# Performance work log

Hardware: AMD Instinct MI355X
Metric: run time of the kernel (lower is better)

The kernel has to match this reference:

```python
import jax, jax.numpy as jnp
import numpy as np

NUM_HEADS = 16
KEY_DIM = 64
B, S, D = 2, 2048, 1024


def setup_inputs() -> dict:
    key = jax.random.key(0)
    ks = jax.random.split(key, 5)
    scale = 1.0 / np.sqrt(D)
    return {
        "x": jax.random.normal(ks[0], (B, S, D), dtype=jnp.float32),
        "Wq": jax.random.normal(ks[1], (D, NUM_HEADS * KEY_DIM), dtype=jnp.float32) * scale,
        "Wk": jax.random.normal(ks[2], (D, NUM_HEADS * KEY_DIM), dtype=jnp.float32) * scale,
        "Wv": jax.random.normal(ks[3], (D, NUM_HEADS * KEY_DIM), dtype=jnp.float32) * scale,
        "Wo": jax.random.normal(ks[4], (NUM_HEADS * KEY_DIM, D), dtype=jnp.float32) * scale,
    }


def reference(x, Wq, Wk, Wv, Wo):
    b, s, d = x.shape
    h, kd = NUM_HEADS, KEY_DIM
    # QKV projections -> [B, H, S, Kd]
    q = (x @ Wq).reshape(b, s, h, kd).transpose(0, 2, 1, 3)
    k = (x @ Wk).reshape(b, s, h, kd).transpose(0, 2, 1, 3)
    v = (x @ Wv).reshape(b, s, h, kd).transpose(0, 2, 1, 3)
    # scaled dot-product attention, full [B,H,S,S] scores (faithful to source)
    logits = jnp.einsum("bhqd,bhkd->bhqk", q, k) / jnp.sqrt(jnp.float32(kd))
    attn = jax.nn.softmax(logits, axis=-1)
    out = jnp.einsum("bhqk,bhkd->bhqd", attn, v)  # [B,H,S,Kd]
    out = out.transpose(0, 2, 1, 3).reshape(b, s, h * kd)
    return out @ Wo
```

## Files before the change

### kernel.cpp

```cpp
#include <hip/hip_runtime.h>


typedef __attribute__((ext_vector_type(8))) short short8;
typedef __attribute__((ext_vector_type(4))) float f32x4;

#define M_ROWS 4096
#define N_COLS 1024
#define K_DIM  1024
#define SEQ    2048

#define QSCALE 0.18033688011111772f

#if defined(__has_builtin)
#if __has_builtin(__builtin_amdgcn_exp2f)
#define EXP2(x) __builtin_amdgcn_exp2f(x)
#endif
#endif
#ifndef EXP2
#define EXP2(x) exp2f(x)
#endif

#define WAITCNT_VM8 0x0F78
#define WAITCNT_VM4 0x0F74

__device__ inline unsigned short f2bf(float f) {
  unsigned int u = __float_as_uint(f);
  u += 0x7fffu + ((u >> 16) & 1u);
  return (unsigned short)(u >> 16);
}

__device__ inline unsigned int pack2bf(float a, float b) {
  unsigned int ua = __float_as_uint(a); ua += 0x7fffu + ((ua >> 16) & 1u);
  unsigned int ub = __float_as_uint(b); ub += 0x7fffu + ((ub >> 16) & 1u);
  return (ua >> 16) | (ub & 0xffff0000u);
}

__device__ inline unsigned int cvtpk(float lo, float hi) {
  unsigned int r;
  asm("v_cvt_pk_bf16_f32 %0, %1, %2" : "=v"(r) : "v"(lo), "v"(hi));
  return r;
}

__device__ inline void swap32(unsigned int& a, unsigned int& b) {
  asm volatile("v_permlane32_swap_b32 %0, %1" : "+v"(a), "+v"(b));
}
__device__ inline void swap16(unsigned int& a, unsigned int& b) {
  asm volatile("v_permlane16_swap_b32 %0, %1" : "+v"(a), "+v"(b));
}

__device__ inline void async_load16(const unsigned short* gptr, unsigned short* lptr) {
  __builtin_amdgcn_global_load_lds(
      (const __attribute__((address_space(1))) unsigned int*)gptr,
      (__attribute__((address_space(3))) unsigned int*)lptr, 16, 0, 0);
}

__global__ void detect_kernel(const unsigned short* __restrict__ x, int* __restrict__ flag) {
  __shared__ int bad;
  if (threadIdx.x == 0) bad = 0;
  __syncthreads();
  for (int i = threadIdx.x; i < 1024; i += 256) {
    float f = __uint_as_float((unsigned int)x[i] << 16);
    float a = fabsf(f);
    if (!(a < 1e4f)) atomicOr(&bad, 1);
  }
  __syncthreads();
  if (threadIdx.x == 0) *flag = bad ? 0 : 1;
}

__global__ void convert_kernel(const void* __restrict__ src, unsigned short* __restrict__ dst,
                               int n4, const int* __restrict__ flag) {
  const int isbf = *flag;
  const int stride = gridDim.x * blockDim.x;
  for (int i = blockIdx.x * blockDim.x + threadIdx.x; i < n4; i += stride) {
    if (isbf) {
      ((uint2*)dst)[i] = ((const uint2*)src)[i];
    } else {
      float4 v = ((const float4*)src)[i];
      ushort4 o;
      o.x = f2bf(v.x); o.y = f2bf(v.y); o.z = f2bf(v.z); o.w = f2bf(v.w);
      ((ushort4*)dst)[i] = o;
    }
  }
}

__global__ __launch_bounds__(256) void convert_wT4_kernel(
    const void* __restrict__ s0, const void* __restrict__ s1,
    const void* __restrict__ s2, const void* __restrict__ s3,
    unsigned short* __restrict__ d0, unsigned short* __restrict__ d1,
    unsigned short* __restrict__ d2, unsigned short* __restrict__ d3,
    const int* __restrict__ flag) {
  __shared__ unsigned short t[32][33];
  const int z = blockIdx.z;
  const void* src = (z == 0) ? s0 : (z == 1) ? s1 : (z == 2) ? s2 : s3;
  unsigned short* dst = (z == 0) ? d0 : (z == 1) ? d1 : (z == 2) ? d2 : d3;
  const int tid = threadIdx.x;
  const int r0 = blockIdx.y * 32, c0 = blockIdx.x * 32;
  const int kr = tid >> 3, nc = (tid & 7) * 4;
  if (*flag) {
    const unsigned short* W = (const unsigned short*)src;
    uint2 v = *(const uint2*)(W + (size_t)(r0 + kr) * K_DIM + c0 + nc);
    t[kr][nc] = v.x & 0xffff; t[kr][nc + 1] = v.x >> 16;
    t[kr][nc + 2] = v.y & 0xffff; t[kr][nc + 3] = v.y >> 16;
  } else {
    const float* W = (const float*)src;
    float4 v = *(const float4*)(W + (size_t)(r0 + kr) * K_DIM + c0 + nc);
    t[kr][nc] = f2bf(v.x); t[kr][nc + 1] = f2bf(v.y);
    t[kr][nc + 2] = f2bf(v.z); t[kr][nc + 3] = f2bf(v.w);
  }
  __syncthreads();
  const int nr = tid >> 3, kc = (tid & 7) * 4;
  uint2 w;
  w.x = (unsigned int)t[kc][nr] | ((unsigned int)t[kc + 1][nr] << 16);
  w.y = (unsigned int)t[kc + 2][nr] | ((unsigned int)t[kc + 3][nr] << 16);
  *(uint2*)(dst + (size_t)(c0 + nr) * K_DIM + r0 + kc) = w;
}

#define GEMM_DMA(Aptr, Bptr, KTOT, KB, BUF)                                       \
  _Pragma("unroll") for (int r = 0; r < 2; ++r) {                                 \
    int s = r * 256 + wave * 64 + lane;                                           \
    int row = s >> 2, c = s & 3;                                                  \
    int g = c ^ ((row ^ (row >> 2)) & 3);                                         \
    async_load16((Aptr) + (size_t)(m0 + row) * (KTOT) + (KB) + g * 8,             \
                 &As[BUF][(size_t)(r * 256 + wave * 64) * 8]);                    \
    async_load16((Bptr) + (size_t)(n0 + row) * (KTOT) + (KB) + g * 8,             \
                 &Bs[BUF][(size_t)(r * 256 + wave * 64) * 8]);                    \
  }

#define GEMM_MAIN_LOOP(Aptr, Bptr, KTOT)                                          \
  f32x4 acc[4][4];                                                                \
  _Pragma("unroll") for (int i = 0; i < 4; ++i)                                   \
  _Pragma("unroll") for (int j = 0; j < 4; ++j)                                   \
      acc[i][j] = (f32x4){0.f, 0.f, 0.f, 0.f};                                    \
  const int xr = (l15 ^ (l15 >> 2)) & 3;                                          \
  GEMM_DMA(Aptr, Bptr, KTOT, 0, 0)                                                \
  for (int kb = 0; kb < (KTOT); kb += 32) {                                       \
    const int pp = (kb >> 5) & 1;                                                 \
    const int kbn = (kb + 32) & ((KTOT) - 1);                                     \
    GEMM_DMA(Aptr, Bptr, KTOT, kbn, pp ^ 1)                                       \
    __builtin_amdgcn_s_waitcnt(WAITCNT_VM4);                                      \
    __syncthreads();                                                              \
    short8 am[4], bn[4];                                                          \
    _Pragma("unroll") for (int i = 0; i < 4; ++i) {                               \
      int arow = wr * 64 + i * 16 + l15;                                          \
      int brow = wc * 64 + i * 16 + l15;                                          \
      int cc = quad ^ xr;                                                         \
      am[i] = *(const short8*)(&As[pp][arow * 32 + cc * 8]);                      \
      bn[i] = *(const short8*)(&Bs[pp][brow * 32 + cc * 8]);                      \
    }                                                                             \
    _Pragma("unroll") for (int i = 0; i < 4; ++i)                                 \
    _Pragma("unroll") for (int j = 0; j < 4; ++j)                                 \
        acc[i][j] = __builtin_amdgcn_mfma_f32_16x16x32_bf16(am[i], bn[j],         \
                                                            acc[i][j], 0, 0, 0); \
    __syncthreads();                                                              \
  }

__global__ __launch_bounds__(256, 3) void qkv_gemm_kernel(
    const unsigned short* __restrict__ Xb,
    const unsigned short* __restrict__ Wqt,
    const unsigned short* __restrict__ Wkt,
    const unsigned short* __restrict__ Wvt,
    unsigned short* __restrict__ Qb,
    unsigned short* __restrict__ Kb,
    unsigned short* __restrict__ Vt) {
  __shared__ __align__(16) unsigned short As[2][128 * 32];
  __shared__ __align__(16) unsigned short Bs[2][128 * 32];
  const int tid = threadIdx.x;
  const int wave = tid >> 6, lane = tid & 63;
  const int quad = lane >> 4, l15 = lane & 15;
  const int wr = wave >> 1, wc = wave & 1;
  const int m0 = blockIdx.x * 128;
  const int n0 = blockIdx.y * 128;
  const int wsel = blockIdx.z;
  const unsigned short* __restrict__ Bt =
      (wsel == 0) ? Wqt : ((wsel == 1) ? Wkt : Wvt);

  GEMM_MAIN_LOOP(Xb, Bt, K_DIM)

#pragma unroll
  for (int i = 0; i < 4; ++i) {
#pragma unroll
    for (int j = 0; j < 4; ++j) {
      int mbase = m0 + wr * 64 + i * 16 + quad * 4;
      int n = n0 + wc * 64 + j * 16 + l15;
      int h = n >> 6, d = n & 63;
      if (wsel == 2) {
        int b_ = mbase >> 11, s = mbase & 2047;
        uint2 w;
        w.x = cvtpk(acc[i][j][0], acc[i][j][1]);
        w.y = cvtpk(acc[i][j][2], acc[i][j][3]);
        *(uint2*)(Vt + ((size_t)(b_ * 16 + h) * 64 + d) * SEQ + s) = w;
      } else {
#pragma unroll
        for (int r = 0; r < 4; ++r) {
          int m = mbase + r;
          int b_ = m >> 11, s = m & 2047;
          float val = acc[i][j][r];
          if (wsel == 0)
            Qb[((size_t)(b_ * 16 + h) * SEQ + s) * 64 + d] = f2bf(val * QSCALE);
          else
            Kb[((size_t)(b_ * 16 + h) * SEQ + s) * 64 + d] = f2bf(val);
        }
      }
    }
  }
}

__global__ __launch_bounds__(256, 2) void flash_kernel(
    const unsigned short* __restrict__ Qb,
    const unsigned short* __restrict__ Kb,
    const unsigned short* __restrict__ Vt,
    unsigned short* __restrict__ Ob) {
  __shared__ __align__(16) unsigned short Klds[2][128 * 64];
  __shared__ __align__(16) unsigned short Vlds[2][64 * 128];
  const int tid = threadIdx.x;
  const int wave = tid >> 6, lane = tid & 63;
  const int quad = lane >> 4, l15 = lane & 15;
  const int gid = blockIdx.x;
  const int bh = gid & 31;
  const int qidx = gid >> 5;
  const int qbase = qidx * 128 + wave * 32;

  const unsigned short* __restrict__ Qp = Qb + (size_t)bh * SEQ * 64;
  const unsigned short* __restrict__ Kp = Kb + (size_t)bh * SEQ * 64;
  const unsigned short* __restrict__ Vp = Vt + (size_t)bh * 64 * SEQ;

  short8 qf[2][2];
#pragma unroll
  for (int g = 0; g < 2; ++g)
#pragma unroll
    for (int h = 0; h < 2; ++h)
      qf[g][h] = *(const short8*)(Qp + (size_t)(qbase + g * 16 + l15) * 64 + h * 32 + quad * 8);

  f32x4 O[2][4];
#pragma unroll
  for (int g = 0; g < 2; ++g)
#pragma unroll
    for (int t = 0; t < 4; ++t) O[g][t] = (f32x4){0.f, 0.f, 0.f, 0.f};
  float l_i[2] = {0.f, 0.f};

#define FLASH_DMA(KB, BUF)                                                     \
  _Pragma("unroll") for (int r = 0; r < 4; ++r) {                              \
    int s = r * 256 + tid;                                                     \
    int krow = s >> 3, kc = s & 7;                                             \
    int kg = kc ^ (krow & 7);                                                  \
    async_load16(Kp + (size_t)((KB) + krow) * 64 + kg * 8,                     \
                 &Klds[BUF][(size_t)(r * 256 + wave * 64) * 8]);               \
    int vrow = s >> 4, vc = s & 15;                                            \
    int vg = vc ^ (vrow & 15);                                                 \
    async_load16(Vp + (size_t)vrow * SEQ + (KB) + vg * 8,                      \
                 &Vlds[BUF][(size_t)(r * 256 + wave * 64) * 8]);               \
  }

  FLASH_DMA(0, 0)

  for (int kb = 0; kb < SEQ; kb += 128) {
    const int p = (kb >> 7) & 1;
    const int kbn = (kb + 128) & (SEQ - 1);
    FLASH_DMA(kbn, p ^ 1)
    __builtin_amdgcn_s_waitcnt(WAITCNT_VM8);
    __syncthreads();

    f32x4 sT[2][8];
    __builtin_amdgcn_s_setprio(1);
#pragma unroll
    for (int t = 0; t < 8; ++t) {
      int row = t * 16 + l15;
      int c0 = quad ^ (row & 7), c1 = (quad + 4) ^ (row & 7);
      short8 k0 = *(const short8*)(&Klds[p][row * 64 + c0 * 8]);
      short8 k1 = *(const short8*)(&Klds[p][row * 64 + c1 * 8]);
      sT[0][t] = __builtin_amdgcn_mfma_f32_16x16x32_bf16(k0, qf[0][0],
                 (f32x4){0.f, 0.f, 0.f, 0.f}, 0, 0, 0);
      sT[0][t] = __builtin_amdgcn_mfma_f32_16x16x32_bf16(k1, qf[0][1], sT[0][t], 0, 0, 0);
      sT[1][t] = __builtin_amdgcn_mfma_f32_16x16x32_bf16(k0, qf[1][0],
                 (f32x4){0.f, 0.f, 0.f, 0.f}, 0, 0, 0);
      sT[1][t] = __builtin_amdgcn_mfma_f32_16x16x32_bf16(k1, qf[1][1], sT[1][t], 0, 0, 0);
    }
    __builtin_amdgcn_s_setprio(0);

    short8 pb[2][4];
#pragma unroll
    for (int g = 0; g < 2; ++g) {
      float rs = 0.f;
      unsigned int wx[8], wy[8];
#pragma unroll
      for (int t = 0; t < 8; ++t) {
        float p0 = EXP2(sT[g][t][0]);
        float p1 = EXP2(sT[g][t][1]);
        float p2 = EXP2(sT[g][t][2]);
        float p3 = EXP2(sT[g][t][3]);
        rs += (p0 + p1) + (p2 + p3);
        wx[t] = cvtpk(p0, p1);
        wy[t] = cvtpk(p2, p3);
      }
      rs += __shfl_xor(rs, 16);
      rs += __shfl_xor(rs, 32);
      l_i[g] += rs;

#pragma unroll
      for (int m = 0; m < 4; ++m) {
        unsigned int a = wx[2 * m], c = wx[2 * m + 1];
        unsigned int b = wy[2 * m], d = wy[2 * m + 1];
        swap32(a, c); swap16(a, c);
        swap32(b, d); swap16(b, d);
        union { short8 s; unsigned int u[4]; } P;
        P.u[0] = a; P.u[1] = b; P.u[2] = c; P.u[3] = d;
        pb[g][m] = P.s;
      }
    }

    __builtin_amdgcn_s_setprio(1);
#pragma unroll
    for (int td = 0; td < 4; ++td) {
      int row = td * 16 + l15;
#pragma unroll
      for (int m = 0; m < 4; ++m) {
        short8 vf = *(const short8*)(&Vlds[p][row * 128 + (((m * 4 + quad) ^ l15) * 8)]);
        O[0][td] = __builtin_amdgcn_mfma_f32_16x16x32_bf16(vf, pb[0][m], O[0][td], 0, 0, 0);
        O[1][td] = __builtin_amdgcn_mfma_f32_16x16x32_bf16(vf, pb[1][m], O[1][td], 0, 0, 0);
      }
    }
    __builtin_amdgcn_s_setprio(0);
    __syncthreads();
  }

  const int b_ = bh >> 4, h = bh & 15;
#pragma unroll
  for (int g = 0; g < 2; ++g) {
    const float inv = 1.f / l_i[g];
    unsigned short* orow = Ob + ((size_t)(b_ * SEQ) + qbase + g * 16 + l15) * N_COLS + h * 64;
#pragma unroll
    for (int t = 0; t < 4; ++t) {
      uint2 w;
      w.x = cvtpk(O[g][t][0] * inv, O[g][t][1] * inv);
      w.y = cvtpk(O[g][t][2] * inv, O[g][t][3] * inv);
      *(uint2*)(orow + t * 16 + quad * 4) = w;
    }
  }
#undef FLASH_DMA
}

__global__ __launch_bounds__(256, 3) void out_gemm_kernel(
    const unsigned short* __restrict__ Ob,
    const unsigned short* __restrict__ Wot,
    void* __restrict__ out,
    const int* __restrict__ flag) {
  __shared__ __align__(16) unsigned short As[2][128 * 32];
  __shared__ __align__(16) unsigned short Bs[2][128 * 32];
  const int tid = threadIdx.x;
  const int wave = tid >> 6, lane = tid & 63;
  const int quad = lane >> 4, l15 = lane & 15;
  const int wr = wave >> 1, wc = wave & 1;
  const int m0 = blockIdx.x * 128;
  const int n0 = blockIdx.y * 128;
  const int isbf = *flag;

  GEMM_MAIN_LOOP(Ob, Wot, N_COLS)

#pragma unroll
  for (int i = 0; i < 4; ++i) {
#pragma unroll
    for (int j = 0; j < 4; ++j) {
      int mbase = m0 + wr * 64 + i * 16 + quad * 4;
      int n = n0 + wc * 64 + j * 16 + l15;
#pragma unroll
      for (int r = 0; r < 4; ++r) {
        float val = acc[i][j][r];
        if (isbf) ((unsigned short*)out)[(size_t)(mbase + r) * K_DIM + n] = f2bf(val);
        else      ((float*)out)[(size_t)(mbase + r) * K_DIM + n] = val;
      }
    }
  }
}

extern "C" void kernel_launch(void* const* d_in, const int* in_sizes, int n_in,
                              void* d_out, int out_size, void* d_ws, size_t ws_size,
                              hipStream_t stream) {
  const void* x  = d_in[0];
  const void* wq = d_in[1];
  const void* wk = d_in[2];
  const void* wv = d_in[3];
  const void* wo = d_in[4];

  char* ws = (char*)d_ws;
  size_t off = 0;
  int* flag = (int*)(ws + off);                 off += 256;
  unsigned short* xb  = (unsigned short*)(ws + off); off += (size_t)M_ROWS * K_DIM * 2;
  unsigned short* wqt = (unsigned short*)(ws + off); off += (size_t)K_DIM * N_COLS * 2;
  unsigned short* wkt = (unsigned short*)(ws + off); off += (size_t)K_DIM * N_COLS * 2;
  unsigned short* wvt = (unsigned short*)(ws + off); off += (size_t)K_DIM * N_COLS * 2;
  unsigned short* wot = (unsigned short*)(ws + off); off += (size_t)N_COLS * K_DIM * 2;
  unsigned short* Qb  = (unsigned short*)(ws + off); off += (size_t)M_ROWS * 1024 * 2;
  unsigned short* Kb  = (unsigned short*)(ws + off); off += (size_t)M_ROWS * 1024 * 2;
  unsigned short* Vtb = (unsigned short*)(ws + off); off += (size_t)M_ROWS * 1024 * 2;
  unsigned short* Ob  = (unsigned short*)(ws + off); off += (size_t)M_ROWS * N_COLS * 2;
  (void)ws_size; (void)in_sizes; (void)n_in; (void)out_size;

  detect_kernel<<<1, 256, 0, stream>>>((const unsigned short*)x, flag);

  convert_kernel<<<2048, 256, 0, stream>>>(x, xb, (M_ROWS * K_DIM) / 4, flag);
  convert_wT4_kernel<<<dim3(32, 32, 4), 256, 0, stream>>>(wq, wk, wv, wo,
                                                          wqt, wkt, wvt, wot, flag);

  qkv_gemm_kernel<<<dim3(32, 8, 3), 256, 0, stream>>>(xb, wqt, wkt, wvt, Qb, Kb, Vtb);
  flash_kernel<<<512, 256, 0, stream>>>(Qb, Kb, Vtb, Ob);
  out_gemm_kernel<<<dim3(32, 8), 256, 0, stream>>>(Ob, wot, d_out, flag);
}
```

Measured before the change: 187.5 us.

## Split flash attention into per-group stages and defer row-sum reduction

The attention inner loop is split by query group. QK^T for group 1 is issued after group 0's scores, and group 0's softmax and PV are interleaved with it so MFMA and exp/VALU work can overlap. The per-block cross-lane shuffle reduction of the softmax row sum is moved out of the key loop and done once at the end. The permlane swaps drop `volatile` so the compiler can schedule them freely. The trade-off is that K fragments are read from LDS twice per block and the register schedule changes.

```diff
diff --git a/kernel.cpp b/kernel.cpp
--- a/kernel.cpp
+++ b/kernel.cpp
@@ -42,10 +42,10 @@
 }
 
 __device__ inline void swap32(unsigned int& a, unsigned int& b) {
-  asm volatile("v_permlane32_swap_b32 %0, %1" : "+v"(a), "+v"(b));
+  asm("v_permlane32_swap_b32 %0, %1" : "+v"(a), "+v"(b));
 }
 __device__ inline void swap16(unsigned int& a, unsigned int& b) {
-  asm volatile("v_permlane16_swap_b32 %0, %1" : "+v"(a), "+v"(b));
+  asm("v_permlane16_swap_b32 %0, %1" : "+v"(a), "+v"(b));
 }
 
 __device__ inline void async_load16(const unsigned short* gptr, unsigned short* lptr) {
@@ -251,6 +251,48 @@
                  &Vlds[BUF][(size_t)(r * 256 + wave * 64) * 8]);               \
   }
 
+#define QK_READ(t)                                                             \
+  int row = (t) * 16 + l15;                                                    \
+  int c0 = quad ^ (row & 7), c1 = (quad + 4) ^ (row & 7);                      \
+  short8 k0 = *(const short8*)(&Klds[p][row * 64 + c0 * 8]);                   \
+  short8 k1 = *(const short8*)(&Klds[p][row * 64 + c1 * 8]);
+
+#define SOFTMAX_G(SRC, PB, G)                                                  \
+  {                                                                            \
+    float rs = 0.f;                                                            \
+    unsigned int wx[8], wy[8];                                                 \
+    _Pragma("unroll") for (int t = 0; t < 8; ++t) {                            \
+      float p0 = EXP2(SRC[t][0]);                                              \
+      float p1 = EXP2(SRC[t][1]);                                              \
+      float p2 = EXP2(SRC[t][2]);                                              \
+      float p3 = EXP2(SRC[t][3]);                                              \
+      rs += (p0 + p1) + (p2 + p3);                                             \
+      wx[t] = cvtpk(p0, p1);                                                   \
+      wy[t] = cvtpk(p2, p3);                                                   \
+    }                                                                          \
+    l_i[G] += rs;                                                              \
+    _Pragma("unroll") for (int m = 0; m < 4; ++m) {                            \
+      unsigned int a = wx[2 * m], c = wx[2 * m + 1];                           \
+      unsigned int b = wy[2 * m], d = wy[2 * m + 1];                           \
+      swap32(a, c); swap16(a, c);                \
+      swap32(b, d); swap16(b, d);                \
+      union { short8 s; unsigned int u[4]; } P;                                \
+      P.u[0] = a; P.u[1] = b; P.u[2] = c; P.u[3] = d;                          \
+      PB[m] = P.s;                                                             \
+    }                                                                          \
+  }
+
+#define PV_G(PB, G)                                                            \
+  _Pragma("unroll") for (int td = 0; td < 4; ++td) {                           \
+    int vrow = td * 16 + l15;                                                  \
+    _Pragma("unroll") for (int m = 0; m < 4; ++m) {                            \
+      short8 vf = *(const short8*)(&Vlds[p][vrow * 128 +                       \
+                                           (((m * 4 + quad) ^ l15) * 8)]);     \
+      O[G][td] = __builtin_amdgcn_mfma_f32_16x16x32_bf16(vf, PB[m],            \
+                                                         O[G][td], 0, 0, 0);   \
+    }                                                                          \
+  }
+
   FLASH_DMA(0, 0)
 
   for (int kb = 0; kb < SEQ; kb += 128) {
@@ -260,67 +302,40 @@
     __builtin_amdgcn_s_waitcnt(WAITCNT_VM8);
     __syncthreads();
 
-    f32x4 sT[2][8];
+    f32x4 sT0[8], sT1[8];
     __builtin_amdgcn_s_setprio(1);
 #pragma unroll
     for (int t = 0; t < 8; ++t) {
-      int row = t * 16 + l15;
-      int c0 = quad ^ (row & 7), c1 = (quad + 4) ^ (row & 7);
-      short8 k0 = *(const short8*)(&Klds[p][row * 64 + c0 * 8]);
-      short8 k1 = *(const short8*)(&Klds[p][row * 64 + c1 * 8]);
-      sT[0][t] = __builtin_amdgcn_mfma_f32_16x16x32_bf16(k0, qf[0][0],
-                 (f32x4){0.f, 0.f, 0.f, 0.f}, 0, 0, 0);
-      sT[0][t] = __builtin_amdgcn_mfma_f32_16x16x32_bf16(k1, qf[0][1], sT[0][t], 0, 0, 0);
-      sT[1][t] = __builtin_amdgcn_mfma_f32_16x16x32_bf16(k0, qf[1][0],
-                 (f32x4){0.f, 0.f, 0.f, 0.f}, 0, 0, 0);
-      sT[1][t] = __builtin_amdgcn_mfma_f32_16x16x32_bf16(k1, qf[1][1], sT[1][t], 0, 0, 0);
+      QK_READ(t)
+      sT0[t] = __builtin_amdgcn_mfma_f32_16x16x32_bf16(k0, qf[0][0],
+               (f32x4){0.f, 0.f, 0.f, 0.f}, 0, 0, 0);
+      sT0[t] = __builtin_amdgcn_mfma_f32_16x16x32_bf16(k1, qf[0][1], sT0[t], 0, 0, 0);
     }
     __builtin_amdgcn_s_setprio(0);
 
-    short8 pb[2][4];
-#pragma unroll
-    for (int g = 0; g < 2; ++g) {
-      float rs = 0.f;
-      unsigned int wx[8], wy[8];
-#pragma unroll
-      for (int t = 0; t < 8; ++t) {
-        float p0 = EXP2(sT[g][t][0]);
-        float p1 = EXP2(sT[g][t][1]);
-        float p2 = EXP2(sT[g][t][2]);
-        float p3 = EXP2(sT[g][t][3]);
-        rs += (p0 + p1) + (p2 + p3);
-        wx[t] = cvtpk(p0, p1);
-        wy[t] = cvtpk(p2, p3);
-      }
-      rs += __shfl_xor(rs, 16);
-      rs += __shfl_xor(rs, 32);
-      l_i[g] += rs;
-
-#pragma unroll
-      for (int m = 0; m < 4; ++m) {
-        unsigned int a = wx[2 * m], c = wx[2 * m + 1];
-        unsigned int b = wy[2 * m], d = wy[2 * m + 1];
-        swap32(a, c); swap16(a, c);
-        swap32(b, d); swap16(b, d);
-        union { short8 s; unsigned int u[4]; } P;
-        P.u[0] = a; P.u[1] = b; P.u[2] = c; P.u[3] = d;
-        pb[g][m] = P.s;
-      }
-    }
-
-    __builtin_amdgcn_s_setprio(1);
-#pragma unroll
-    for (int td = 0; td < 4; ++td) {
-      int row = td * 16 + l15;
-#pragma unroll
-      for (int m = 0; m < 4; ++m) {
-        short8 vf = *(const short8*)(&Vlds[p][row * 128 + (((m * 4 + quad) ^ l15) * 8)]);
-        O[0][td] = __builtin_amdgcn_mfma_f32_16x16x32_bf16(vf, pb[0][m], O[0][td], 0, 0, 0);
-        O[1][td] = __builtin_amdgcn_mfma_f32_16x16x32_bf16(vf, pb[1][m], O[1][td], 0, 0, 0);
-      }
-    }
-    __builtin_amdgcn_s_setprio(0);
+#pragma unroll
+    for (int t = 0; t < 8; ++t) {
+      QK_READ(t)
+      sT1[t] = __builtin_amdgcn_mfma_f32_16x16x32_bf16(k0, qf[1][0],
+               (f32x4){0.f, 0.f, 0.f, 0.f}, 0, 0, 0);
+      sT1[t] = __builtin_amdgcn_mfma_f32_16x16x32_bf16(k1, qf[1][1], sT1[t], 0, 0, 0);
+    }
+    short8 pb0[4];
+    SOFTMAX_G(sT0, pb0, 0)
+
+    PV_G(pb0, 0)
+    short8 pb1[4];
+    SOFTMAX_G(sT1, pb1, 1)
+
+    PV_G(pb1, 1)
+
     __syncthreads();
+  }
+
+#pragma unroll
+  for (int g = 0; g < 2; ++g) {
+    l_i[g] += __shfl_xor(l_i[g], 16);
+    l_i[g] += __shfl_xor(l_i[g], 32);
   }
 
   const int b_ = bh >> 4, h = bh & 15;
@@ -337,6 +352,9 @@
     }
   }
 #undef FLASH_DMA
+#undef QK_READ
+#undef SOFTMAX_G
+#undef PV_G
 }
 
 __global__ __launch_bounds__(256, 3) void out_gemm_kernel(
```

Result: no change. 187.5 us (+0.0%).
